# Optimization experiments

Hardware: AMD Instinct MI355X
Metric: run time of the kernel (lower is better)

## Reference

```python
import jax, jax.numpy as jnp
import numpy as np

# dims matching init_kwargs
E, TOPK, H, DK, DV, D = 4, 2, 8, 64, 64, 512
B, L = 4, 1024
VDIM = H * DV  # value_dim = key_dim * expand_v (expand_v=1.0)


def _silu(x):
    return x * jax.nn.sigmoid(x)


def _l2norm(x):
    return x * jax.lax.rsqrt(jnp.sum(x * x, axis=-1, keepdims=True) + 1e-6)


def setup_inputs() -> dict:
    key = jax.random.key(0)
    ks = jax.random.split(key, 12)
    std = 0.02
    h = jax.random.normal(ks[0], (B, L, D), jnp.float32)
    Wq = jax.random.normal(ks[1], (D, H * DK), jnp.float32) * std
    Wgate = jax.random.normal(ks[2], (D, E), jnp.float32) * std
    Wk = jax.random.normal(ks[3], (D, H * DK), jnp.float32) * std
    Wv = jax.random.normal(ks[4], (D, VDIM), jnp.float32) * std
    Wb = jax.random.normal(ks[5], (D, H), jnp.float32) * std
    Wa = jax.random.normal(ks[6], (D, H), jnp.float32) * std
    Wg = jax.random.normal(ks[7], (D, VDIM), jnp.float32) * std
    Wo = jax.random.normal(ks[8], (VDIM, D), jnp.float32) * std
    A = jax.random.uniform(ks[9], (H,), jnp.float32, 1e-4, 16.0)
    A_log = jnp.log(A)
    dt = jnp.exp(jax.random.uniform(ks[10], (H,), jnp.float32) * (np.float32(np.log(0.1)) - np.float32(np.log(0.001))) + np.float32(np.log(0.001)))
    dt = jnp.maximum(dt, 1e-4)
    dt_bias = dt + jnp.log(-jnp.expm1(-dt))
    o_norm_weight = jnp.ones((DV,), jnp.float32)
    return {"hidden_states": h, "Wq": Wq, "Wgate": Wgate, "Wk": Wk, "Wv": Wv,
            "Wb": Wb, "Wa": Wa, "A_log": A_log, "dt_bias": dt_bias, "Wg": Wg,
            "o_norm_weight": o_norm_weight, "Wo": Wo}


def _forward(h, Wq, Wgate, Wk, Wv, Wb, Wa, A_log, dt_bias, Wg, o_norm_weight, Wo):
    Bs, Ls, _ = h.shape
    # router: softmax -> topk -> renormalize -> scatter to full [B,L,E]
    scores = jax.nn.softmax((h @ Wgate).astype(jnp.float32), axis=-1)
    rw, sel = jax.lax.top_k(scores, TOPK)
    rw = rw / jnp.sum(rw, axis=-1, keepdims=True)
    bi = jnp.arange(Bs)[:, None, None]
    li = jnp.arange(Ls)[None, :, None]
    w_full = jnp.zeros((Bs, Ls, E), jnp.float32).at[bi, li, sel].set(rw)
    m = jnp.transpose(w_full > 0, (2, 0, 1))  # [E,B,L] routing mask

    # shared projections (single_kv_proj=True); silu feature map, qk l2-norm
    q = _l2norm(_silu(h @ Wq).reshape(Bs, Ls, H, DK))
    k = _l2norm(_silu(h @ Wk).reshape(Bs, Ls, H, DK))
    v = _silu(h @ Wv).reshape(Bs, Ls, H, DV)
    beta = jax.nn.sigmoid(h @ Wb)  # [B,L,H]
    g = -jnp.exp(A_log) * jax.nn.softplus((h @ Wa).astype(jnp.float32) + dt_bias)  # [B,L,H]

    # dispatch-equivalent masking: non-routed tokens get beta=0, g=0 so the
    # per-memory state is unchanged there (same math as compact gather+pad)
    beta_e = beta[None] * m[..., None]          # [E,B,L,H]
    g_e = jnp.where(m[..., None], g[None], 0.0)  # [E,B,L,H]

    scale = DK ** -0.5
    xs = (jnp.moveaxis(q, 1, 0), jnp.moveaxis(k, 1, 0), jnp.moveaxis(v, 1, 0),
          jnp.moveaxis(beta_e, 2, 0), jnp.moveaxis(g_e, 2, 0))

    def step(S, x):  # S: [E,B,H,DK,DV]
        qt, kt, vt, bt, gt = x
        S = S * jnp.exp(gt)[..., None, None]
        kv = jnp.einsum('bhk,ebhkv->ebhv', kt, S)
        delta = (vt[None] - kv) * bt[..., None]
        S = S + kt[None, :, :, :, None] * delta[..., None, :]
        ot = jnp.einsum('bhk,ebhkv->ebhv', qt * scale, S)
        return S, ot

    S0 = jnp.zeros((E, Bs, H, DK, DV), jnp.float32)
    _, o = jax.lax.scan(step, S0, xs)   # [L,E,B,H,DV]
    o = jnp.moveaxis(o, 0, 2)            # [E,B,L,H,DV]

    # weighted scatter-combine across memories
    core = jnp.einsum('ble,eblhv->blhv', w_full, o)

    # FusedRMSNormGated + output projection
    gate = _silu((h @ Wg).reshape(Bs, Ls, H, DV))
    core = core * jax.lax.rsqrt(jnp.mean(core * core, axis=-1, keepdims=True) + 1e-5)
    core = core * o_norm_weight * gate
    return core.reshape(Bs, Ls, VDIM) @ Wo


def reference(hidden_states, Wq, Wgate, Wk, Wv, Wb, Wa, A_log, dt_bias, Wg, o_norm_weight, Wo):
    return _forward(hidden_states, Wq, Wgate, Wk, Wv, Wb, Wa, A_log, dt_bias, Wg, o_norm_weight, Wo)
```

## Files before the change

kernel.cpp:

```cpp
#include <hip/hip_runtime.h>
#include <math.h>

#define DMODEL 512
#define NHEADS 8
#define NEXP 4
#define SEQ 1024
#define BATCH 4
#define NTOK 4096
#define NCHUNK 16

typedef float v2f __attribute__((ext_vector_type(2)));
typedef float v4f __attribute__((ext_vector_type(4)));
typedef short bf16x8 __attribute__((ext_vector_type(8)));
typedef float f32x4 __attribute__((ext_vector_type(4)));
typedef unsigned short u16;

__device__ __forceinline__ float dev_sigmoid(float x) { return 1.0f / (1.0f + expf(-x)); }
__device__ __forceinline__ float dev_silu(float x) { return x / (1.0f + expf(-x)); }
__device__ __forceinline__ float dev_softplus(float x) {
  return x > 0.0f ? x + log1pf(expf(-x)) : log1pf(expf(x));
}
__device__ __forceinline__ u16 f2b(float f) {
  unsigned int u = __float_as_uint(f);
  unsigned int r = (u + 0x7fffu + ((u >> 16) & 1u)) >> 16;
  return (u16)r;
}
__device__ __forceinline__ ushort4 f2b4(float4 v) {
  ushort4 o; o.x = f2b(v.x); o.y = f2b(v.y); o.z = f2b(v.z); o.w = f2b(v.w); return o;
}

#define BST 72

__global__ __launch_bounds__(256) void zero_kernel(float4* __restrict__ p) {
  p[(size_t)blockIdx.x * 256 + threadIdx.x] = make_float4(0.f, 0.f, 0.f, 0.f);
}

__global__ __launch_bounds__(256) void cast_h_kernel(const float4* __restrict__ in,
                                                     ushort4* __restrict__ outp) {
  const size_t i = (size_t)blockIdx.x * 256 + threadIdx.x;
  outp[i] = f2b4(in[i]);
}

__global__ __launch_bounds__(256) void castT_kernel(const float* __restrict__ in,
                                                    u16* __restrict__ outp) {
  __shared__ float tile[32][33];
  const int bx = blockIdx.x * 32;
  const int by = blockIdx.y * 32;
  const int c = threadIdx.x & 31, r0 = threadIdx.x >> 5;
#pragma unroll
  for (int r = r0; r < 32; r += 8) tile[r][c] = in[(size_t)(bx + r) * DMODEL + by + c];
  __syncthreads();
#pragma unroll
  for (int r = r0; r < 32; r += 8)
    outp[(size_t)(by + r) * DMODEL + bx + c] = f2b(tile[c][r]);
}

__global__ __launch_bounds__(256) void kT_kernel(const float* __restrict__ kb,
                                                 u16* __restrict__ ktg) {
  const int ch = blockIdx.x, b = blockIdx.y, hh = blockIdx.z;
  const int tile = (b * NHEADS + hh) * NCHUNK + ch;
  const int tid = threadIdx.x;
  __shared__ float tl[64][65];
  {
    const int t = tid >> 2, d0 = (tid & 3) * 16;
    const float* krow = kb + (size_t)(b * SEQ + ch * 64 + t) * DMODEL + hh * 64 + d0;
#pragma unroll
    for (int j = 0; j < 4; ++j) {
      float4 v = *(const float4*)(krow + j * 4);
      tl[t][d0 + j * 4 + 0] = v.x; tl[t][d0 + j * 4 + 1] = v.y;
      tl[t][d0 + j * 4 + 2] = v.z; tl[t][d0 + j * 4 + 3] = v.w;
    }
  }
  __syncthreads();
  {
    const int t = tid & 63, dk0 = (tid >> 6) * 16;
    u16* obase = ktg + (size_t)tile * 4096 + t;
#pragma unroll
    for (int j = 0; j < 16; ++j)
      obase[(size_t)(dk0 + j) * 64] = f2b(tl[t][dk0 + j]);
  }
}

__global__ __launch_bounds__(64) void router_kernel(
    const float* __restrict__ h, const float* __restrict__ Wb,
    const float* __restrict__ Wa, const float* __restrict__ Wgate,
    const float* __restrict__ A_log, const float* __restrict__ dt_bias,
    float* __restrict__ beta_o, float* __restrict__ g_o, float* __restrict__ w_o) {
  const int t = blockIdx.x;
  const int lane = threadIdx.x;
  float hv[8];
#pragma unroll
  for (int j = 0; j < 8; ++j) hv[j] = h[(size_t)t * DMODEL + j * 64 + lane];
  float db[8], da[8], dg[4];
#pragma unroll
  for (int c = 0; c < 8; ++c) {
    float s1 = 0.f, s2 = 0.f;
#pragma unroll
    for (int j = 0; j < 8; ++j) {
      int row = j * 64 + lane;
      s1 += hv[j] * Wb[row * NHEADS + c];
      s2 += hv[j] * Wa[row * NHEADS + c];
    }
#pragma unroll
    for (int off = 1; off < 64; off <<= 1) {
      s1 += __shfl_xor(s1, off);
      s2 += __shfl_xor(s2, off);
    }
    db[c] = s1; da[c] = s2;
  }
#pragma unroll
  for (int c = 0; c < 4; ++c) {
    float s = 0.f;
#pragma unroll
    for (int j = 0; j < 8; ++j) s += hv[j] * Wgate[(j * 64 + lane) * NEXP + c];
#pragma unroll
    for (int off = 1; off < 64; off <<= 1) s += __shfl_xor(s, off);
    dg[c] = s;
  }
  if (lane == 0) {
#pragma unroll
    for (int c = 0; c < 8; ++c) {
      beta_o[t * NHEADS + c] = dev_sigmoid(db[c]);
      g_o[t * NHEADS + c] = -expf(A_log[c]) * dev_softplus(da[c] + dt_bias[c]);
    }
    float mx = fmaxf(fmaxf(dg[0], dg[1]), fmaxf(dg[2], dg[3]));
    float p[4]; float sum = 0.f;
#pragma unroll
    for (int c = 0; c < 4; ++c) { p[c] = expf(dg[c] - mx); sum += p[c]; }
#pragma unroll
    for (int c = 0; c < 4; ++c) p[c] /= sum;
    float v1 = -1e30f; int i1 = 0;
#pragma unroll
    for (int c = 0; c < 4; ++c) { if (p[c] > v1) { v1 = p[c]; i1 = c; } }
    float v2 = -1e30f; int i2 = -1;
#pragma unroll
    for (int c = 0; c < 4; ++c) { if (c != i1 && p[c] > v2) { v2 = p[c]; i2 = c; } }
    float s2v = v1 + v2;
#pragma unroll
    for (int c = 0; c < 4; ++c) {
      float wv = 0.f;
      if (c == i1) wv = v1 / s2v;
      else if (c == i2) wv = v2 / s2v;
      w_o[t * NEXP + c] = wv;
    }
  }
}

__global__ __launch_bounds__(64) void compact_kernel(
    const float* __restrict__ wbuf, int* __restrict__ tidx, int* __restrict__ tcnt) {
  const int e = blockIdx.x, b = blockIdx.y;
  const int lane = threadIdx.x;
  int* out = tidx + (e * BATCH + b) * SEQ;
  int cnt = 0;
  for (int g0 = 0; g0 < SEQ; g0 += 64) {
    const int l = g0 + lane;
    const float w = wbuf[(b * SEQ + l) * NEXP + e];
    const unsigned long long m = __ballot(w > 0.f);
    const int pos = __popcll(m & ((1ull << lane) - 1ull));
    if (w > 0.f) out[cnt + pos] = l;
    cnt += __popcll(m);
  }
  if (lane == 0) tcnt[e * BATCH + b] = cnt;
}

#define LDA 56
template <int MODE>
__global__ __launch_bounds__(128) void gemm_mfma(
    const u16* __restrict__ A, const u16* __restrict__ Bt,
    float* __restrict__ C) {
  constexpr int K = DMODEL, N = DMODEL;
  __shared__ __align__(16) short As[128 * LDA];
  __shared__ __align__(16) short Bs[64 * LDA];
  const int tid = threadIdx.x;
  const int wave = tid >> 6, lane = tid & 63;
  const int quad = lane >> 4, l16 = lane & 15;
  const int m0 = blockIdx.x * 128, n0 = blockIdx.y * 64;
  const int bn = tid >> 1, bk = (tid & 1) * 16;
  const u16* Abase = A + (size_t)(m0 + tid) * K;
  const u16* Bbase = Bt + (size_t)(n0 + bn) * K + bk;

  f32x4 acc[4][4];
#pragma unroll
  for (int i = 0; i < 4; ++i)
#pragma unroll
    for (int j = 0; j < 4; ++j) acc[i][j] = (f32x4){0.f, 0.f, 0.f, 0.f};

  int4 pa0, pa1, pa2, pa3, pb0, pb1;
  {
    const u16* p = Abase;
    pa0 = *(const int4*)p; pa1 = *(const int4*)(p + 8);
    pa2 = *(const int4*)(p + 16); pa3 = *(const int4*)(p + 24);
    const u16* q = Bbase;
    pb0 = *(const int4*)q; pb1 = *(const int4*)(q + 8);
  }
  for (int kk = 0; kk < K; kk += 32) {
    __syncthreads();
    *(int4*)&As[tid * LDA + 0] = pa0;
    *(int4*)&As[tid * LDA + 8] = pa1;
    *(int4*)&As[tid * LDA + 16] = pa2;
    *(int4*)&As[tid * LDA + 24] = pa3;
    *(int4*)&Bs[bn * LDA + bk] = pb0;
    *(int4*)&Bs[bn * LDA + bk + 8] = pb1;
    __syncthreads();
    if (kk + 32 < K) {
      const u16* p = Abase + kk + 32;
      pa0 = *(const int4*)p; pa1 = *(const int4*)(p + 8);
      pa2 = *(const int4*)(p + 16); pa3 = *(const int4*)(p + 24);
      const u16* q = Bbase + kk + 32;
      pb0 = *(const int4*)q; pb1 = *(const int4*)(q + 8);
    }
    bf16x8 af[4], bfg[4];
#pragma unroll
    for (int mi = 0; mi < 4; ++mi)
      af[mi] = *(const bf16x8*)&As[(wave * 64 + mi * 16 + l16) * LDA + quad * 8];
#pragma unroll
    for (int ni = 0; ni < 4; ++ni)
      bfg[ni] = *(const bf16x8*)&Bs[(ni * 16 + l16) * LDA + quad * 8];
#pragma unroll
    for (int mi = 0; mi < 4; ++mi)
#pragma unroll
      for (int ni = 0; ni < 4; ++ni)
        acc[mi][ni] = __builtin_amdgcn_mfma_f32_16x16x32_bf16(af[mi], bfg[ni],
                                                              acc[mi][ni], 0, 0, 0);
  }
#pragma unroll
  for (int mi = 0; mi < 4; ++mi) {
#pragma unroll
    for (int r = 0; r < 4; ++r) {
      const int row = m0 + wave * 64 + mi * 16 + quad * 4 + r;
      float s[4];
#pragma unroll
      for (int ni = 0; ni < 4; ++ni) {
        float x = acc[mi][ni][r];
        s[ni] = (MODE == 0) ? x : dev_silu(x);
      }
      if (MODE == 2) {
        float ss = s[0] * s[0] + s[1] * s[1] + s[2] * s[2] + s[3] * s[3];
        ss += __shfl_xor(ss, 1);
        ss += __shfl_xor(ss, 2);
        ss += __shfl_xor(ss, 4);
        ss += __shfl_xor(ss, 8);
        const float rn = 1.0f / sqrtf(ss + 1e-6f);
#pragma unroll
        for (int ni = 0; ni < 4; ++ni) s[ni] *= rn;
      }
#pragma unroll
      for (int ni = 0; ni < 4; ++ni)
        C[(size_t)row * N + n0 + ni * 16 + l16] = s[ni];
    }
  }
}


__global__ __launch_bounds__(256) void chunk_phase1(
    const float* __restrict__ kb, const float* __restrict__ vb,
    const float* __restrict__ betab, const float* __restrict__ gbuf,
    const float* __restrict__ wbuf, float* __restrict__ U0buf,
    float* __restrict__ Wbuf, float* __restrict__ cbuf) {
  const int ch = blockIdx.x, eb = blockIdx.y, hh = blockIdx.z;
  const int e = eb >> 2, b = eb & 3;
  const int chunkid = (eb * NHEADS + hh) * NCHUNK + ch;
  const size_t base = (size_t)chunkid * 4096;
  const int tid = threadIdx.x;
  const int wave = tid >> 6, lane = tid & 63;
  const int quad = lane >> 4, l16 = lane & 15;

  __shared__ __align__(16) short Kb[64 * BST];
  __shared__ __align__(16) short Tb[64 * BST];
  __shared__ float Td[4][16][17];
  __shared__ __align__(16) short Xt[128 * BST];
  __shared__ float Zl[16][136];
  __shared__ float cc[64], bb[64], exs[64];

  if (tid < 64) {
    const int gt = b * SEQ + ch * 64 + tid;
    const float w = wbuf[gt * NEXP + e];
    float gv = 0.f, bv = 0.f;
    if (w > 0.f) { gv = gbuf[gt * NHEADS + hh]; bv = betab[gt * NHEADS + hh]; }
    float cum = gv;
#pragma unroll
    for (int off = 1; off < 64; off <<= 1) {
      float o = __shfl_up(cum, off);
      if (tid >= off) cum += o;
    }
    cc[tid] = cum; exs[tid] = expf(cum); bb[tid] = bv;
    cbuf[(size_t)chunkid * 64 + tid] = cum;
  }
#pragma unroll
  for (int i = tid; i < 64 * 32; i += 256)
    ((int*)&Tb[(i >> 5) * BST])[i & 31] = 0;
#pragma unroll
  for (int i = tid; i < 128 * 32; i += 256)
    ((int*)&Xt[(i >> 5) * BST])[i & 31] = 0;
  {
    const int t = tid >> 2, d0 = (tid & 3) * 16;
    const float* krow = kb + (size_t)(b * SEQ + ch * 64 + t) * DMODEL + hh * 64 + d0;
#pragma unroll
    for (int j = 0; j < 4; ++j)
      *(ushort4*)&Kb[t * BST + d0 + j * 4] = f2b4(*(const float4*)(krow + j * 4));
  }
  __syncthreads();
  for (int ni = 0; ni <= wave; ++ni) {
    f32x4 acc = (f32x4){0.f, 0.f, 0.f, 0.f};
#pragma unroll
    for (int ks = 0; ks < 2; ++ks) {
      bf16x8 af = *(const bf16x8*)&Kb[(wave * 16 + l16) * BST + ks * 32 + quad * 8];
      bf16x8 bfr = *(const bf16x8*)&Kb[(ni * 16 + l16) * BST + ks * 32 + quad * 8];
      acc = __builtin_amdgcn_mfma_f32_16x16x32_bf16(af, bfr, acc, 0, 0, 0);
    }
#pragma unroll
    for (int r = 0; r < 4; ++r) {
      const int t = wave * 16 + quad * 4 + r, s = ni * 16 + l16;
      if (s < t) {
        const float val = bb[t] * expf(cc[t] - cc[s]) * acc[r];
        if (ni == wave) Td[wave][t & 15][s & 15] = val;
        else Tb[t * BST + s] = f2b(val);
      }
    }
  }
  __syncthreads();

  const bool solver = tid < 128;
  const bool isV = tid < 64;
  const int col = tid & 63;
  const float* src = isV ? vb : kb;
  const size_t srow = (size_t)(b * SEQ + ch * 64) * DMODEL + hh * 64 + col;
  float u[16];

#pragma unroll
  for (int p = 0; p < 4; ++p) {
    if (p > 0) {
      const int nch = (p + 1) >> 1;
      f32x4 a0 = (f32x4){0.f, 0.f, 0.f, 0.f};
      f32x4 a1 = (f32x4){0.f, 0.f, 0.f, 0.f};
      for (int ks = 0; ks < nch; ++ks) {
        bf16x8 af = *(const bf16x8*)&Tb[(p * 16 + l16) * BST + ks * 32 + quad * 8];
        bf16x8 b0 = *(const bf16x8*)&Xt[(wave * 32 + l16) * BST + ks * 32 + quad * 8];
        bf16x8 b1 = *(const bf16x8*)&Xt[(wave * 32 + 16 + l16) * BST + ks * 32 + quad * 8];
        a0 = __builtin_amdgcn_mfma_f32_16x16x32_bf16(af, b0, a0, 0, 0, 0);
        a1 = __builtin_amdgcn_mfma_f32_16x16x32_bf16(af, b1, a1, 0, 0, 0);
      }
#pragma unroll
      for (int r = 0; r < 4; ++r) {
        Zl[quad * 4 + r][wave * 32 + l16] = a0[r];
        Zl[quad * 4 + r][wave * 32 + 16 + l16] = a1[r];
      }
      __syncthreads();
    }
    if (solver) {
#pragma unroll
      for (int i = 0; i < 16; ++i) {
        const int t = p * 16 + i;
        const float R = src[srow + (size_t)t * DMODEL];
        const float sc = isV ? bb[t] : bb[t] * exs[t];
        float v0 = sc * R - ((p > 0) ? Zl[i][tid] : 0.f);
        float v1 = 0.f;
#pragma unroll
        for (int r = 0; r < i; ++r) {
          if (r & 1) v1 = fmaf(-Td[p][i][r], u[r], v1);
          else       v0 = fmaf(-Td[p][i][r], u[r], v0);
        }
        u[i] = v0 + v1;
      }
#pragma unroll
      for (int j = 0; j < 4; ++j) {
        ushort4 o;
        o.x = f2b(u[j * 4 + 0]); o.y = f2b(u[j * 4 + 1]);
        o.z = f2b(u[j * 4 + 2]); o.w = f2b(u[j * 4 + 3]);
        *(ushort4*)&Xt[tid * BST + p * 16 + j * 4] = o;
      }
      if (isV) {
        float* dst = U0buf + base + (size_t)col * 64 + p * 16;
#pragma unroll
        for (int j = 0; j < 4; ++j)
          *(float4*)(dst + j * 4) = make_float4(u[j * 4], u[j * 4 + 1], u[j * 4 + 2], u[j * 4 + 3]);
      } else {
        float* dst = Wbuf + base + col;
#pragma unroll
        for (int i = 0; i < 16; ++i) dst[(size_t)(p * 16 + i) * 64] = u[i];
      }
    }
    __syncthreads();
  }
}

__global__ __launch_bounds__(256) void chunk_phase2(
    const float* __restrict__ cbuf, const float* __restrict__ U0buf,
    const float* __restrict__ Wbuf, const u16* __restrict__ ktg,
    u16* __restrict__ Utg, u16* __restrict__ Stg) {
  const int eb = blockIdx.x, hh = blockIdx.y;
  const int b = eb & 3;
  const int ebh = eb * NHEADS + hh;
  const int tid = threadIdx.x;
  const int wave = tid >> 6, lane = tid & 63;
  const int quad = lane >> 4, l16 = lane & 15;

  __shared__ float Sf[64][68];
  __shared__ __align__(16) short Sbt[64 * BST];
  __shared__ __align__(16) short Wb[64 * BST];
  __shared__ __align__(16) short Ktb[64 * BST];
  __shared__ __align__(16) short UextT[64 * BST];
  __shared__ float ext[64];
  __shared__ float gamS;

  for (int i = tid; i < 64 * 68; i += 256) (&Sf[0][0])[i] = 0.f;
  __syncthreads();

  const int ktile0 = (b * NHEADS + hh) * NCHUNK;

  for (int ch = 0; ch < NCHUNK; ++ch) {
    const int chunkid = ebh * NCHUNK + ch;
    const size_t base = (size_t)chunkid * 4096;
    const size_t kbase = (size_t)(ktile0 + ch) * 4096;
    if (tid < 64) {
      const float cv = cbuf[(size_t)chunkid * 64 + tid];
      const float c63 = __shfl(cv, 63);
      ext[tid] = expf(c63 - cv);
      if (tid == 63) gamS = expf(cv);
    }
    {
      const int r = tid >> 2, c0 = (tid & 3) * 16;
      const float* wrow = Wbuf + base + (size_t)r * 64 + c0;
      const u16* krow = ktg + kbase + (size_t)r * 64 + c0;
#pragma unroll
      for (int j = 0; j < 4; ++j) {
        *(ushort4*)&Wb[r * BST + c0 + j * 4] = f2b4(*(const float4*)(wrow + j * 4));
        *(ushort4*)&Ktb[r * BST + c0 + j * 4] = *(const ushort4*)(krow + j * 4);
      }
    }
    for (int i = tid; i < 1024; i += 256) {
      const int dv = i >> 4, d4 = (i & 15) * 4;
      const float* s4 = &Sf[dv][d4];
      ushort4 o; o.x = f2b(s4[0]); o.y = f2b(s4[1]); o.z = f2b(s4[2]); o.w = f2b(s4[3]);
      *(ushort4*)&Sbt[dv * BST + d4] = o;
    }
    __syncthreads();
    for (int i = tid; i < 1024; i += 256) {
      const int r = i >> 4, c4 = (i & 15) * 4;
      *(ushort4*)(Stg + base + r * 64 + c4) = *(const ushort4*)&Sbt[r * BST + c4];
    }
    for (int ni = 0; ni < 4; ++ni) {
      f32x4 acc = (f32x4){0.f, 0.f, 0.f, 0.f};
#pragma unroll
      for (int ks = 0; ks < 2; ++ks) {
        bf16x8 af = *(const bf16x8*)&Sbt[(wave * 16 + l16) * BST + ks * 32 + quad * 8];
        bf16x8 bfr = *(const bf16x8*)&Wb[(ni * 16 + l16) * BST + ks * 32 + quad * 8];
        acc = __builtin_amdgcn_mfma_f32_16x16x32_bf16(af, bfr, acc, 0, 0, 0);
      }
#pragma unroll
      for (int r = 0; r < 4; ++r) {
        const int dv = wave * 16 + quad * 4 + r, t = ni * 16 + l16;
        const float uv = U0buf[base + (size_t)dv * 64 + t] - acc[r];
        Utg[base + (size_t)dv * 64 + t] = f2b(uv);
        UextT[dv * BST + t] = f2b(uv * ext[t]);
      }
    }
    __syncthreads();
    const float g = gamS;
    for (int ni = 0; ni < 4; ++ni) {
      f32x4 acc = (f32x4){0.f, 0.f, 0.f, 0.f};
#pragma unroll
      for (int ks = 0; ks < 2; ++ks) {
        bf16x8 af = *(const bf16x8*)&UextT[(wave * 16 + l16) * BST + ks * 32 + quad * 8];
        bf16x8 bfr = *(const bf16x8*)&Ktb[(ni * 16 + l16) * BST + ks * 32 + quad * 8];
        acc = __builtin_amdgcn_mfma_f32_16x16x32_bf16(af, bfr, acc, 0, 0, 0);
      }
#pragma unroll
      for (int r = 0; r < 4; ++r) {
        const int dv = wave * 16 + quad * 4 + r, dk = ni * 16 + l16;
        Sf[dv][dk] = g * Sf[dv][dk] + acc[r];
      }
    }
    __syncthreads();
  }
}

__global__ __launch_bounds__(256) void chunk_phase3(
    const float* __restrict__ qb, const float* __restrict__ kb,
    const float* __restrict__ cbuf, const u16* __restrict__ Utg,
    const u16* __restrict__ Stg, const float* __restrict__ wbuf,
    float* __restrict__ coreb) {
  const int ch = blockIdx.x, eb = blockIdx.y, hh = blockIdx.z;
  const int e = eb >> 2, b = eb & 3;
  const int chunkid = (eb * NHEADS + hh) * NCHUNK + ch;
  const size_t base = (size_t)chunkid * 4096;
  const int tid = threadIdx.x;
  const int wave = tid >> 6, lane = tid & 63;
  const int quad = lane >> 4, l16 = lane & 15;

  __shared__ __align__(16) short Qb[64 * BST];
  __shared__ __align__(16) short Kb3[64 * BST];
  __shared__ __align__(16) short Pb[64 * BST];
  __shared__ __align__(16) short Stb[64 * BST];
  __shared__ __align__(16) short Utb[64 * BST];
  __shared__ float cc3[64];

  if (tid < 64) cc3[tid] = cbuf[(size_t)chunkid * 64 + tid];
  {
    const int t = tid >> 2, d0 = (tid & 3) * 16;
    const size_t ro = (size_t)(b * SEQ + ch * 64 + t) * DMODEL + hh * 64 + d0;
#pragma unroll
    for (int j = 0; j < 4; ++j) {
      *(ushort4*)&Qb[t * BST + d0 + j * 4] = f2b4(*(const float4*)(qb + ro + j * 4));
      *(ushort4*)&Kb3[t * BST + d0 + j * 4] = f2b4(*(const float4*)(kb + ro + j * 4));
    }
  }
  for (int i = tid; i < 1024; i += 256) {
    const int r = i >> 4, c4 = (i & 15) * 4;
    *(ushort4*)&Stb[r * BST + c4] = *(const ushort4*)(Stg + base + r * 64 + c4);
    *(ushort4*)&Utb[r * BST + c4] = *(const ushort4*)(Utg + base + r * 64 + c4);
  }
  __syncthreads();
  for (int ni = 0; ni < 4; ++ni) {
    f32x4 acc = (f32x4){0.f, 0.f, 0.f, 0.f};
#pragma unroll
    for (int ks = 0; ks < 2; ++ks) {
      bf16x8 af = *(const bf16x8*)&Qb[(wave * 16 + l16) * BST + ks * 32 + quad * 8];
      bf16x8 bfr = *(const bf16x8*)&Kb3[(ni * 16 + l16) * BST + ks * 32 + quad * 8];
      acc = __builtin_amdgcn_mfma_f32_16x16x32_bf16(af, bfr, acc, 0, 0, 0);
    }
#pragma unroll
    for (int r = 0; r < 4; ++r) {
      const int t = wave * 16 + quad * 4 + r, s = ni * 16 + l16;
      const float p = (s <= t) ? expf(cc3[t] - cc3[s]) * acc[r] : 0.f;
      Pb[t * BST + s] = f2b(p);
    }
  }
  __syncthreads();
  for (int ni = 0; ni < 4; ++ni) {
    f32x4 a1 = (f32x4){0.f, 0.f, 0.f, 0.f};
    f32x4 a2 = (f32x4){0.f, 0.f, 0.f, 0.f};
#pragma unroll
    for (int ks = 0; ks < 2; ++ks) {
      bf16x8 afq = *(const bf16x8*)&Qb[(wave * 16 + l16) * BST + ks * 32 + quad * 8];
      bf16x8 bfs = *(const bf16x8*)&Stb[(ni * 16 + l16) * BST + ks * 32 + quad * 8];
      a1 = __builtin_amdgcn_mfma_f32_16x16x32_bf16(afq, bfs, a1, 0, 0, 0);
      bf16x8 afp = *(const bf16x8*)&Pb[(wave * 16 + l16) * BST + ks * 32 + quad * 8];
      bf16x8 bfu = *(const bf16x8*)&Utb[(ni * 16 + l16) * BST + ks * 32 + quad * 8];
      a2 = __builtin_amdgcn_mfma_f32_16x16x32_bf16(afp, bfu, a2, 0, 0, 0);
    }
#pragma unroll
    for (int r = 0; r < 4; ++r) {
      const int t = wave * 16 + quad * 4 + r, dv = ni * 16 + l16;
      const int gt = b * SEQ + ch * 64 + t;
      const float wv = wbuf[gt * NEXP + e];
      if (wv > 0.f) {
        const float o = 0.125f * (expf(cc3[t]) * a1[r] + a2[r]);
        atomicAdd(&coreb[(size_t)gt * DMODEL + hh * 64 + dv], wv * o);
      }
    }
  }
}

__global__ __launch_bounds__(64) void scan_kernel(
    const float* __restrict__ qb, const float* __restrict__ kb,
    const float* __restrict__ vb, const float* __restrict__ betab,
    const float* __restrict__ gbuf, const float* __restrict__ wbuf,
    const int* __restrict__ tidx, const int* __restrict__ tcnt,
    float* __restrict__ coreb) {
  const int vhalf = blockIdx.x & 1, e = blockIdx.x >> 1;
  const int b = blockIdx.y, hh = blockIdx.z;
  const int lane = threadIdx.x;
  const int kh = lane >> 5;
  const int vi = lane & 31;
  const int cv = vhalf * 32 + vi;
  const int* idx = tidx + (e * BATCH + b) * SEQ;
  const int n = tcnt[e * BATCH + b];
  if (n == 0) return;
  const int nm1 = n - 1;
  __shared__ __align__(16) float lk[4][64];
  __shared__ __align__(16) float lq[4][64];
  __shared__ int lidx[SEQ];
  for (int i = lane; i < SEQ; i += 64) lidx[i] = idx[i < n ? i : nm1];
  __syncthreads();
  v2f S2[16];
#pragma unroll
  for (int j = 0; j < 16; ++j) S2[j] = (v2f){0.f, 0.f};
  float kf[4], qf[4], vf[4], gf[4], bf[4], wf[4], egr[4];
  int tcur[4], tok4[4];
#define PREF(SLOT, TK)                                          \
  do {                                                          \
    const int tn_ = b * SEQ + (TK);                             \
    const size_t kq_ = (size_t)tn_ * DMODEL + hh * 64 + lane;   \
    kf[SLOT] = kb[kq_];                                         \
    qf[SLOT] = qb[kq_];                                         \
    vf[SLOT] = vb[(size_t)tn_ * DMODEL + hh * 64 + cv];         \
    gf[SLOT] = gbuf[tn_ * NHEADS + hh];                         \
    bf[SLOT] = betab[tn_ * NHEADS + hh];                        \
    wf[SLOT] = wbuf[tn_ * NEXP + e];                            \
    tcur[SLOT] = tn_;                                           \
  } while (0)
  tok4[0] = lidx[0];
  tok4[1] = lidx[1 < n ? 1 : nm1];
  tok4[2] = lidx[2 < n ? 2 : nm1];
  tok4[3] = lidx[3 < n ? 3 : nm1];
  PREF(0, tok4[0]); PREF(1, tok4[1]); PREF(2, tok4[2]);
  lk[0][lane] = kf[0]; lq[0][lane] = qf[0];
  egr[0] = expf(gf[0]);
  const int m = (n + 3) & ~3;
  for (int i = 0; i < m; i += 4) {
#pragma unroll
    for (int u = 0; u < 4; ++u) {
      const int s = i + u;
      const int sN = (u + 3) & 3;
      const int s1 = (u + 1) & 3;
      PREF(sN, tok4[sN]);
      int a4 = s + 4;
      a4 = a4 < nm1 ? a4 : nm1;
      tok4[u] = lidx[a4];
      __builtin_amdgcn_wave_barrier();
      lk[s1][lane] = kf[s1];
      lq[s1][lane] = qf[s1];
      __builtin_amdgcn_wave_barrier();
      egr[s1] = expf(gf[s1]);
      const v4f* lk4 = (const v4f*)&lk[u][kh * 32];
      const v4f* lq4 = (const v4f*)&lq[u][kh * 32];
      v2f myk[16];
      v2f c0 = (v2f){0.f, 0.f}, c1 = c0, c2 = c0, c3 = c0;
#pragma unroll
      for (int j = 0; j < 8; ++j) {
        const v4f k4 = lk4[j];
        const v2f klo = (v2f){k4.x, k4.y};
        const v2f khi = (v2f){k4.z, k4.w};
        myk[2 * j] = klo; myk[2 * j + 1] = khi;
        if (j & 1) {
          c2 = __builtin_elementwise_fma(klo, S2[2 * j], c2);
          c3 = __builtin_elementwise_fma(khi, S2[2 * j + 1], c3);
        } else {
          c0 = __builtin_elementwise_fma(klo, S2[2 * j], c0);
          c1 = __builtin_elementwise_fma(khi, S2[2 * j + 1], c1);
        }
      }
      const v2f cacc = (c0 + c1) + (c2 + c3);
      float cd = cacc.x + cacc.y;
      cd += __shfl_xor(cd, 32);
      const float egc = egr[u];
      const float delta = (vf[u] - egc * cd) * bf[u];
      const v2f d2 = (v2f){delta, delta};
      const v2f eg2 = (v2f){egc, egc};
      v2f o0 = (v2f){0.f, 0.f}, o1 = o0, o2 = o0, o3 = o0;
#pragma unroll
      for (int j = 0; j < 8; ++j) {
        const v4f q4 = lq4[j];
        const v2f qlo = (v2f){q4.x, q4.y};
        const v2f qhi = (v2f){q4.z, q4.w};
        const v2f s0 = __builtin_elementwise_fma(S2[2 * j], eg2, myk[2 * j] * d2);
        const v2f s1v = __builtin_elementwise_fma(S2[2 * j + 1], eg2, myk[2 * j + 1] * d2);
        S2[2 * j] = s0; S2[2 * j + 1] = s1v;
        if (j & 1) {
          o2 = __builtin_elementwise_fma(qlo, s0, o2);
          o3 = __builtin_elementwise_fma(qhi, s1v, o3);
        } else {
          o0 = __builtin_elementwise_fma(qlo, s0, o0);
          o1 = __builtin_elementwise_fma(qhi, s1v, o1);
        }
      }
      const v2f oacc = (o0 + o1) + (o2 + o3);
      float o = oacc.x + oacc.y;
      o += __shfl_xor(o, 32);
      if (kh == 0 && s < n)
        atomicAdd(&coreb[(size_t)tcur[u] * DMODEL + hh * 64 + cv],
                  o * 0.125f * wf[u]);
    }
  }
#undef PREF
}

__global__ __launch_bounds__(512) void rmsnorm_kernel(
    const float* __restrict__ coreb, const float* __restrict__ gateb,
    const float* __restrict__ wn, u16* __restrict__ outb) {
  const int t = blockIdx.x;
  const int tid = threadIdx.x;
  const int v = tid & 63;
  const float x = coreb[(size_t)t * DMODEL + tid];
  float ss = x * x;
#pragma unroll
  for (int off = 1; off < 64; off <<= 1) ss += __shfl_xor(ss, off);
  const float r = rsqrtf(ss * (1.0f / 64.0f) + 1e-5f);
  const float gt = gateb[(size_t)t * DMODEL + tid];
  outb[(size_t)t * DMODEL + tid] = f2b(x * r * wn[v] * gt);
}

extern "C" void kernel_launch(void* const* d_in, const int* in_sizes, int n_in,
                              void* d_out, int out_size, void* d_ws, size_t ws_size,
                              hipStream_t stream) {
  const float* h       = (const float*)d_in[0];
  const float* Wq      = (const float*)d_in[1];
  const float* Wgate   = (const float*)d_in[2];
  const float* Wk      = (const float*)d_in[3];
  const float* Wv      = (const float*)d_in[4];
  const float* Wb      = (const float*)d_in[5];
  const float* Wa      = (const float*)d_in[6];
  const float* A_log   = (const float*)d_in[7];
  const float* dt_bias = (const float*)d_in[8];
  const float* Wg      = (const float*)d_in[9];
  const float* wn      = (const float*)d_in[10];
  const float* Wo      = (const float*)d_in[11];
  float* out = (float*)d_out;

  char* p = (char*)d_ws;
  const size_t big = (size_t)NTOK * DMODEL;
  auto alloc = [&](size_t bytes) { char* r = p; p += (bytes + 255) & ~255ull; return r; };
  float* qb    = (float*)alloc(big * 4);
  float* kb    = (float*)alloc(big * 4);
  float* vb    = (float*)alloc(big * 4);
  float* gateb = (float*)alloc(big * 4);
  float* coreb = (float*)alloc(big * 4);
  float* betab = (float*)alloc((size_t)NTOK * NHEADS * 4);
  float* gbuf  = (float*)alloc((size_t)NTOK * NHEADS * 4);
  float* wbuf  = (float*)alloc((size_t)NTOK * NEXP * 4);
  int*   tidx  = (int*)alloc((size_t)NEXP * BATCH * SEQ * 4);
  int*   tcnt  = (int*)alloc(256);
  u16*   hb    = (u16*)alloc(big * 2);
  u16*   nb    = (u16*)alloc(big * 2);
  u16*   wtq   = (u16*)alloc((size_t)DMODEL * DMODEL * 2);
  u16*   wtk   = (u16*)alloc((size_t)DMODEL * DMODEL * 2);
  u16*   wtv   = (u16*)alloc((size_t)DMODEL * DMODEL * 2);
  u16*   wtg   = (u16*)alloc((size_t)DMODEL * DMODEL * 2);
  u16*   wto   = (u16*)alloc((size_t)DMODEL * DMODEL * 2);
  const size_t nchunks = (size_t)NEXP * BATCH * NHEADS * NCHUNK;
  float* U0buf = (float*)alloc(nchunks * 4096 * 4);
  float* Wbuf_ = (float*)alloc(nchunks * 4096 * 4);
  u16*   Utg   = (u16*)alloc(nchunks * 4096 * 2);
  u16*   Stg   = (u16*)alloc(nchunks * 4096 * 2);
  float* cbuf  = (float*)alloc(nchunks * 64 * 4);
  u16*   ktg   = (u16*)alloc((size_t)BATCH * NHEADS * NCHUNK * 4096 * 2);
  const size_t need = (size_t)(p - (char*)d_ws);
  const bool use_chunked = (ws_size >= need);

  zero_kernel<<<dim3(NTOK * DMODEL / 4 / 256), 256, 0, stream>>>((float4*)coreb);

  cast_h_kernel<<<dim3(big / 4 / 256), 256, 0, stream>>>((const float4*)h, (ushort4*)hb);
  dim3 tg(16, 16);
  castT_kernel<<<tg, 256, 0, stream>>>(Wq, wtq);
  castT_kernel<<<tg, 256, 0, stream>>>(Wk, wtk);
  castT_kernel<<<tg, 256, 0, stream>>>(Wv, wtv);
  castT_kernel<<<tg, 256, 0, stream>>>(Wg, wtg);
  castT_kernel<<<tg, 256, 0, stream>>>(Wo, wto);

  router_kernel<<<dim3(NTOK), 64, 0, stream>>>(h, Wb, Wa, Wgate, A_log, dt_bias,
                                               betab, gbuf, wbuf);

  dim3 gg(NTOK / 128, DMODEL / 64);
  gemm_mfma<2><<<gg, 128, 0, stream>>>(hb, wtq, qb);
  gemm_mfma<2><<<gg, 128, 0, stream>>>(hb, wtk, kb);
  gemm_mfma<1><<<gg, 128, 0, stream>>>(hb, wtv, vb);
  gemm_mfma<1><<<gg, 128, 0, stream>>>(hb, wtg, gateb);

  if (use_chunked) {
    kT_kernel<<<dim3(NCHUNK, BATCH, NHEADS), 256, 0, stream>>>(kb, ktg);
    chunk_phase1<<<dim3(NCHUNK, NEXP * BATCH, NHEADS), 256, 0, stream>>>(
        kb, vb, betab, gbuf, wbuf, U0buf, Wbuf_, cbuf);
    chunk_phase2<<<dim3(NEXP * BATCH, NHEADS), 256, 0, stream>>>(
        cbuf, U0buf, Wbuf_, ktg, Utg, Stg);
    chunk_phase3<<<dim3(NCHUNK, NEXP * BATCH, NHEADS), 256, 0, stream>>>(
        qb, kb, cbuf, Utg, Stg, wbuf, coreb);
  } else {
    compact_kernel<<<dim3(NEXP, BATCH), 64, 0, stream>>>(wbuf, tidx, tcnt);
    scan_kernel<<<dim3(NEXP * 2, BATCH, NHEADS), 64, 0, stream>>>(
        qb, kb, vb, betab, gbuf, wbuf, tidx, tcnt, coreb);
  }

  rmsnorm_kernel<<<dim3(NTOK), 512, 0, stream>>>(coreb, gateb, wn, nb);

  gemm_mfma<0><<<gg, 128, 0, stream>>>(nb, wto, out);
}
```

Baseline: 317.5 us.

## Split phase2 state recurrence across DV halves and prefetch next chunk into registers

```diff
diff --git a/kernel.cpp b/kernel.cpp
--- a/kernel.cpp
+++ b/kernel.cpp
@@ -388,91 +388,122 @@
     const float* __restrict__ cbuf, const float* __restrict__ U0buf,
     const float* __restrict__ Wbuf, const u16* __restrict__ ktg,
     u16* __restrict__ Utg, u16* __restrict__ Stg) {
-  const int eb = blockIdx.x, hh = blockIdx.y;
+  const int eb = blockIdx.x, hh = blockIdx.y, dvh = blockIdx.z;
   const int b = eb & 3;
   const int ebh = eb * NHEADS + hh;
   const int tid = threadIdx.x;
   const int wave = tid >> 6, lane = tid & 63;
   const int quad = lane >> 4, l16 = lane & 15;
-
-  __shared__ float Sf[64][68];
-  __shared__ __align__(16) short Sbt[64 * BST];
+  const int mi = wave >> 1;
+  const int nb0 = (wave & 1) * 2;
+  const int dvl0 = mi * 16 + quad * 4;
+  const int dvg0 = dvh * 32;
+
+  __shared__ float Sf[32][68];
+  __shared__ __align__(16) short Sbt[32 * BST];
   __shared__ __align__(16) short Wb[64 * BST];
   __shared__ __align__(16) short Ktb[64 * BST];
-  __shared__ __align__(16) short UextT[64 * BST];
+  __shared__ __align__(16) short UextT[32 * BST];
   __shared__ float ext[64];
-  __shared__ float gamS;
-
-  for (int i = tid; i < 64 * 68; i += 256) (&Sf[0][0])[i] = 0.f;
+  __shared__ float gam_sh;
+
+  for (int i = tid; i < 32 * 68; i += 256) (&Sf[0][0])[i] = 0.f;
+
+  const int ktile0 = (b * NHEADS + hh) * NCHUNK;
+  const int sr = tid >> 2, sc = (tid & 3) * 16;
+
+  float4 wreg[4];
+  int4 ktreg[2];
+  float u0cur[2][4], u0nxt[2][4];
+  float cvreg;
+
+#define P2_PREF(CH, WD, KD, UD, CV)                                          \
+  do {                                                                       \
+    const int ch_ = (CH) < NCHUNK ? (CH) : (NCHUNK - 1);                     \
+    const size_t b_ = (size_t)(ebh * NCHUNK + ch_) * 4096;                   \
+    const size_t kb_ = (size_t)(ktile0 + ch_) * 4096;                        \
+    const float* wr_ = Wbuf + b_ + (size_t)sr * 64 + sc;                     \
+    WD[0] = *(const float4*)(wr_ + 0);  WD[1] = *(const float4*)(wr_ + 4);   \
+    WD[2] = *(const float4*)(wr_ + 8);  WD[3] = *(const float4*)(wr_ + 12);  \
+    const u16* kr_ = ktg + kb_ + (size_t)sr * 64 + sc;                       \
+    KD[0] = *(const int4*)kr_; KD[1] = *(const int4*)(kr_ + 8);              \
+    _Pragma("unroll")                                                        \
+    for (int ni_ = 0; ni_ < 2; ++ni_)                                        \
+      _Pragma("unroll")                                                      \
+      for (int r_ = 0; r_ < 4; ++r_)                                         \
+        UD[ni_][r_] = U0buf[b_ + (size_t)(dvg0 + dvl0 + r_) * 64 +           \
+                            (nb0 + ni_) * 16 + l16];                         \
+    CV = cbuf[(size_t)(ebh * NCHUNK + ch_) * 64 + (tid & 63)];               \
+  } while (0)
+
+  P2_PREF(0, wreg, ktreg, u0cur, cvreg);
   __syncthreads();
 
-  const int ktile0 = (b * NHEADS + hh) * NCHUNK;
-
   for (int ch = 0; ch < NCHUNK; ++ch) {
-    const int chunkid = ebh * NCHUNK + ch;
-    const size_t base = (size_t)chunkid * 4096;
-    const size_t kbase = (size_t)(ktile0 + ch) * 4096;
+    const size_t base = (size_t)(ebh * NCHUNK + ch) * 4096;
     if (tid < 64) {
-      const float cv = cbuf[(size_t)chunkid * 64 + tid];
-      const float c63 = __shfl(cv, 63);
-      ext[tid] = expf(c63 - cv);
-      if (tid == 63) gamS = expf(cv);
-    }
-    {
-      const int r = tid >> 2, c0 = (tid & 3) * 16;
-      const float* wrow = Wbuf + base + (size_t)r * 64 + c0;
-      const u16* krow = ktg + kbase + (size_t)r * 64 + c0;
-#pragma unroll
-      for (int j = 0; j < 4; ++j) {
-        *(ushort4*)&Wb[r * BST + c0 + j * 4] = f2b4(*(const float4*)(wrow + j * 4));
-        *(ushort4*)&Ktb[r * BST + c0 + j * 4] = *(const ushort4*)(krow + j * 4);
-      }
-    }
-    for (int i = tid; i < 1024; i += 256) {
+      const float c63 = __shfl(cvreg, 63);
+      ext[tid] = expf(c63 - cvreg);
+      if (tid == 63) gam_sh = expf(cvreg);
+    }
+#pragma unroll
+    for (int j = 0; j < 4; ++j)
+      *(ushort4*)&Wb[sr * BST + sc + j * 4] = f2b4(wreg[j]);
+    *(int4*)&Ktb[sr * BST + sc] = ktreg[0];
+    *(int4*)&Ktb[sr * BST + sc + 8] = ktreg[1];
+    for (int i = tid; i < 512; i += 256) {
       const int dv = i >> 4, d4 = (i & 15) * 4;
       const float* s4 = &Sf[dv][d4];
       ushort4 o; o.x = f2b(s4[0]); o.y = f2b(s4[1]); o.z = f2b(s4[2]); o.w = f2b(s4[3]);
       *(ushort4*)&Sbt[dv * BST + d4] = o;
     }
     __syncthreads();
-    for (int i = tid; i < 1024; i += 256) {
+    P2_PREF(ch + 1, wreg, ktreg, u0nxt, cvreg);
+    for (int i = tid; i < 512; i += 256) {
       const int r = i >> 4, c4 = (i & 15) * 4;
-      *(ushort4*)(Stg + base + r * 64 + c4) = *(const ushort4*)&Sbt[r * BST + c4];
-    }
-    for (int ni = 0; ni < 4; ++ni) {
+      *(ushort4*)(Stg + base + (size_t)(dvg0 + r) * 64 + c4) = *(const ushort4*)&Sbt[r * BST + c4];
+    }
+#pragma unroll
+    for (int ni = 0; ni < 2; ++ni) {
       f32x4 acc = (f32x4){0.f, 0.f, 0.f, 0.f};
 #pragma unroll
       for (int ks = 0; ks < 2; ++ks) {
-        bf16x8 af = *(const bf16x8*)&Sbt[(wave * 16 + l16) * BST + ks * 32 + quad * 8];
-        bf16x8 bfr = *(const bf16x8*)&Wb[(ni * 16 + l16) * BST + ks * 32 + quad * 8];
+        bf16x8 af = *(const bf16x8*)&Sbt[(mi * 16 + l16) * BST + ks * 32 + quad * 8];
+        bf16x8 bfr = *(const bf16x8*)&Wb[((nb0 + ni) * 16 + l16) * BST + ks * 32 + quad * 8];
         acc = __builtin_amdgcn_mfma_f32_16x16x32_bf16(af, bfr, acc, 0, 0, 0);
       }
 #pragma unroll
       for (int r = 0; r < 4; ++r) {
-        const int dv = wave * 16 + quad * 4 + r, t = ni * 16 + l16;
-        const float uv = U0buf[base + (size_t)dv * 64 + t] - acc[r];
-        Utg[base + (size_t)dv * 64 + t] = f2b(uv);
-        UextT[dv * BST + t] = f2b(uv * ext[t]);
+        const int dvl = dvl0 + r, t = (nb0 + ni) * 16 + l16;
+        const float uv = u0cur[ni][r] - acc[r];
+        Utg[base + (size_t)(dvg0 + dvl) * 64 + t] = f2b(uv);
+        UextT[dvl * BST + t] = f2b(uv * ext[t]);
       }
     }
     __syncthreads();
-    const float g = gamS;
-    for (int ni = 0; ni < 4; ++ni) {
+    const float g = gam_sh;
+#pragma unroll
+    for (int ni = 0; ni < 2; ++ni) {
       f32x4 acc = (f32x4){0.f, 0.f, 0.f, 0.f};
 #pragma unroll
       for (int ks = 0; ks < 2; ++ks) {
-        bf16x8 af = *(const bf16x8*)&UextT[(wave * 16 + l16) * BST + ks * 32 + quad * 8];
-        bf16x8 bfr = *(const bf16x8*)&Ktb[(ni * 16 + l16) * BST + ks * 32 + quad * 8];
+        bf16x8 af = *(const bf16x8*)&UextT[(mi * 16 + l16) * BST + ks * 32 + quad * 8];
+        bf16x8 bfr = *(const bf16x8*)&Ktb[((nb0 + ni) * 16 + l16) * BST + ks * 32 + quad * 8];
         acc = __builtin_amdgcn_mfma_f32_16x16x32_bf16(af, bfr, acc, 0, 0, 0);
       }
 #pragma unroll
       for (int r = 0; r < 4; ++r) {
-        const int dv = wave * 16 + quad * 4 + r, dk = ni * 16 + l16;
-        Sf[dv][dk] = g * Sf[dv][dk] + acc[r];
-      }
-    }
+        const int dvl = dvl0 + r, dk = (nb0 + ni) * 16 + l16;
+        Sf[dvl][dk] = g * Sf[dvl][dk] + acc[r];
+      }
+    }
+#pragma unroll
+    for (int ni = 0; ni < 2; ++ni)
+#pragma unroll
+      for (int r = 0; r < 4; ++r) u0cur[ni][r] = u0nxt[ni][r];
     __syncthreads();
   }
+#undef P2_PREF
 }
 
 __global__ __launch_bounds__(256) void chunk_phase3(
@@ -751,7 +782,7 @@
     kT_kernel<<<dim3(NCHUNK, BATCH, NHEADS), 256, 0, stream>>>(kb, ktg);
     chunk_phase1<<<dim3(NCHUNK, NEXP * BATCH, NHEADS), 256, 0, stream>>>(
         kb, vb, betab, gbuf, wbuf, U0buf, Wbuf_, cbuf);
-    chunk_phase2<<<dim3(NEXP * BATCH, NHEADS), 256, 0, stream>>>(
+    chunk_phase2<<<dim3(NEXP * BATCH, NHEADS, 2), 256, 0, stream>>>(
         cbuf, U0buf, Wbuf_, ktg, Utg, Stg);
     chunk_phase3<<<dim3(NCHUNK, NEXP * BATCH, NHEADS), 256, 0, stream>>>(
         qb, kb, cbuf, Utg, Stg, wbuf, coreb);
```

Result: faster. 308.5 us (-2.8%).
